# Performance work log

Hardware: AMD Instinct MI355X
Metric: run time of the kernel (lower is better)

Reference implementation:

```python
import jax, jax.numpy as jnp
import numpy as np

B, T, H = 64, 2048, 256
NEG_INF = -10.0 ** 10  # matches torch code's -10**10 pad value


def setup_inputs() -> dict:
    key = jax.random.key(0)
    k1, k2, k3, k4, k5 = jax.random.split(key, 5)
    questions = jax.random.normal(k1, (B, T, H), dtype=jnp.float32)
    questions_lens = jax.random.randint(k2, (B,), 1, T + 1)  # lengths in [1, T]
    W = jax.random.normal(k3, (H, H), dtype=jnp.float32) * (1.0 / np.sqrt(H))
    b = jax.random.normal(k4, (H,), dtype=jnp.float32) * 0.02
    v = jax.random.normal(k5, (H,), dtype=jnp.float32) * (1.0 / np.sqrt(H))
    return {"questions": questions, "questions_lens": questions_lens, "W": W, "b": b, "v": v}


def reference(questions, questions_lens, W, b, v):
    # energy[b,t] = v . (W @ q[b,t] + b)  -- batched instead of per-token loop
    # = (q @ W^T) @ v + (b . v)
    energies = jnp.einsum('bth,h->bt', jnp.einsum('bth,kh->btk', questions, W) + b, v)
    t_idx = jnp.arange(questions.shape[1])  # [T]
    mask = t_idx[None, :] < questions_lens[:, None]  # [B,T] valid positions
    energies = jnp.where(mask, energies, NEG_INF)
    return jax.nn.softmax(energies, axis=1)
```

## Files before the change

kernel.cpp:

```cpp
#include <hip/hip_runtime.h>

constexpr int B_ = 64;
constexpr int T_ = 2048;
constexpr int H_ = 256;
constexpr float NEGINF = -1e10f;

__global__ __launch_bounds__(256) void prep_kernel(
    const float* __restrict__ W, const float* __restrict__ v,
    float* __restrict__ partial) {
  const int h = threadIdx.x;
  const int j = blockIdx.x;
  float acc = 0.f;
#pragma unroll 8
  for (int kk = 0; kk < 64; ++kk) {
    const int k = j * 64 + kk;
    acc = fmaf(v[k], W[k * H_ + h], acc);
  }
  partial[j * H_ + h] = acc;
}

__global__ __launch_bounds__(256) void energy_kernel(
    const float4* __restrict__ q4, const int* __restrict__ lens,
    const float4* __restrict__ p4,
    float* __restrict__ e) {
  const int bb = blockIdx.y;
  const int t0 = blockIdx.x * 256;
  const int len = lens[bb];
  const int tid = threadIdx.x;
  float* erow = e + (size_t)bb * T_;

  if (t0 >= len) {
    erow[t0 + tid] = NEGINF;
    return;
  }

  const int tg = tid >> 3;
  const int c4 = tid & 7;

  float4 uf[8];
#pragma unroll
  for (int hh = 0; hh < 8; ++hh) {
    float4 s = p4[hh * 8 + c4];
#pragma unroll
    for (int j = 1; j < 4; ++j) {
      const float4 t = p4[j * 64 + hh * 8 + c4];
      s.x += t.x; s.y += t.y; s.z += t.z; s.w += t.w;
    }
    uf[hh] = s;
  }

  const float4* qbase =
      q4 + ((size_t)bb * T_ + t0 + tg) * (H_ / 4) + c4;

  float acc[8];
#pragma unroll
  for (int i = 0; i < 8; ++i) acc[i] = 0.f;

#pragma unroll
  for (int i = 0; i < 8; ++i) {
    const int t = t0 + tg + 32 * i;
    if (t < len) {
      const float4* qp = qbase + (size_t)i * 32 * (H_ / 4);
#pragma unroll
      for (int hh = 0; hh < 8; ++hh) {
        const float4 qv = qp[hh * 8];
        acc[i] = fmaf(qv.x, uf[hh].x, acc[i]);
        acc[i] = fmaf(qv.y, uf[hh].y, acc[i]);
        acc[i] = fmaf(qv.z, uf[hh].z, acc[i]);
        acc[i] = fmaf(qv.w, uf[hh].w, acc[i]);
      }
    }
  }

#pragma unroll
  for (int off = 1; off < 8; off <<= 1) {
#pragma unroll
    for (int i = 0; i < 8; ++i) acc[i] += __shfl_xor(acc[i], off);
  }

  float val = 0.f;
#pragma unroll
  for (int k = 0; k < 8; ++k)
    if (c4 == k) val = acc[k];
  const int t = t0 + tg + 32 * c4;
  erow[t] = (t < len) ? val : NEGINF;
}

__global__ __launch_bounds__(256) void softmax_kernel(
    const float* __restrict__ e, float* __restrict__ out) {
  const int bb = blockIdx.x;
  const int tid = threadIdx.x;
  const int wave = tid >> 6;
  const int lane = tid & 63;
  const float* erow = e + (size_t)bb * T_;
  float* orow = out + (size_t)bb * T_;

  float vals[T_ / 256];
  float m = NEGINF;
#pragma unroll
  for (int i = 0; i < T_ / 256; ++i) {
    vals[i] = erow[i * 256 + tid];
    m = fmaxf(m, vals[i]);
  }
#pragma unroll
  for (int off = 32; off > 0; off >>= 1) m = fmaxf(m, __shfl_xor(m, off));

  __shared__ float sm[4];
  __shared__ float ssum[4];
  if (lane == 0) sm[wave] = m;
  __syncthreads();
  m = fmaxf(fmaxf(sm[0], sm[1]), fmaxf(sm[2], sm[3]));

  float s = 0.f;
#pragma unroll
  for (int i = 0; i < T_ / 256; ++i) {
    vals[i] = expf(vals[i] - m);
    s += vals[i];
  }
#pragma unroll
  for (int off = 32; off > 0; off >>= 1) s += __shfl_xor(s, off);
  if (lane == 0) ssum[wave] = s;
  __syncthreads();
  s = ssum[0] + ssum[1] + ssum[2] + ssum[3];
  const float inv = 1.f / s;
#pragma unroll
  for (int i = 0; i < T_ / 256; ++i) orow[i * 256 + tid] = vals[i] * inv;
}

extern "C" void kernel_launch(void* const* d_in, const int* in_sizes, int n_in,
                              void* d_out, int out_size, void* d_ws,
                              size_t ws_size, hipStream_t stream) {
  const float* q = (const float*)d_in[0];
  const int* lens = (const int*)d_in[1];
  const float* W = (const float*)d_in[2];
  const float* v = (const float*)d_in[4];
  float* out = (float*)d_out;

  char* ws = (char*)d_ws;
  float* partial = (float*)ws;
  float* e = (float*)(ws + 8192);

  prep_kernel<<<dim3(4), dim3(256), 0, stream>>>(W, v, partial);
  energy_kernel<<<dim3(T_ / 256, B_), dim3(256), 0, stream>>>(
      (const float4*)q, lens, (const float4*)partial, e);
  softmax_kernel<<<dim3(B_), dim3(256), 0, stream>>>(e, out);
}
```

Before: 192.3 us.

## Fuse W^T v prep, energy and softmax into one kernel with last-block reduction

Merges the three kernels into a single launch. Each active block recomputes u = W^T v into shared memory, computes its tile of energies, then atomically bumps a per-row counter; the last block to finish a row does that row's softmax. A fast path drops per-row bounds checks for fully valid tiles. This removes two launches and inter-kernel gaps, but adds a memset, redundant W reads of 256 KB per active block, and a serial softmax tail on the last block of each row.

```diff
diff --git a/kernel.cpp b/kernel.cpp
--- a/kernel.cpp
+++ b/kernel.cpp
@@ -5,94 +5,99 @@
 constexpr int H_ = 256;
 constexpr float NEGINF = -1e10f;
 
-__global__ __launch_bounds__(256) void prep_kernel(
+__global__ __launch_bounds__(256) void fused_kernel(
+    const float4* __restrict__ q4, const int* __restrict__ lens,
     const float* __restrict__ W, const float* __restrict__ v,
-    float* __restrict__ partial) {
-  const int h = threadIdx.x;
-  const int j = blockIdx.x;
-  float acc = 0.f;
-#pragma unroll 8
-  for (int kk = 0; kk < 64; ++kk) {
-    const int k = j * 64 + kk;
-    acc = fmaf(v[k], W[k * H_ + h], acc);
-  }
-  partial[j * H_ + h] = acc;
-}
-
-__global__ __launch_bounds__(256) void energy_kernel(
-    const float4* __restrict__ q4, const int* __restrict__ lens,
-    const float4* __restrict__ p4,
-    float* __restrict__ e) {
+    float* __restrict__ e, unsigned int* __restrict__ row_cnt,
+    float* __restrict__ out) {
   const int bb = blockIdx.y;
   const int t0 = blockIdx.x * 256;
+  const int tid = threadIdx.x;
   const int len = lens[bb];
-  const int tid = threadIdx.x;
   float* erow = e + (size_t)bb * T_;
 
-  if (t0 >= len) {
+  __shared__ float su[H_];
+  __shared__ int s_last;
+
+  if (t0 < len) {
+    float uacc = 0.f;
+#pragma unroll 8
+    for (int k = 0; k < H_; ++k) uacc = fmaf(v[k], W[k * H_ + tid], uacc);
+    su[tid] = uacc;
+    __syncthreads();
+
+    const int tg = tid >> 3;
+    const int c4 = tid & 7;
+    float4 uf[8];
+#pragma unroll
+    for (int hh = 0; hh < 8; ++hh)
+      uf[hh] = reinterpret_cast<const float4*>(su)[hh * 8 + c4];
+
+    const float4* qbase =
+        q4 + ((size_t)bb * T_ + t0 + tg) * (H_ / 4) + c4;
+
+    float acc[8];
+#pragma unroll
+    for (int i = 0; i < 8; ++i) acc[i] = 0.f;
+
+    if (t0 + 256 <= len) {
+#pragma unroll
+      for (int i = 0; i < 8; ++i) {
+        const float4* qp = qbase + (size_t)i * 32 * (H_ / 4);
+#pragma unroll
+        for (int hh = 0; hh < 8; ++hh) {
+          const float4 qv = qp[hh * 8];
+          acc[i] = fmaf(qv.x, uf[hh].x, acc[i]);
+          acc[i] = fmaf(qv.y, uf[hh].y, acc[i]);
+          acc[i] = fmaf(qv.z, uf[hh].z, acc[i]);
+          acc[i] = fmaf(qv.w, uf[hh].w, acc[i]);
+        }
+      }
+    } else {
+#pragma unroll
+      for (int i = 0; i < 8; ++i) {
+        const int t = t0 + tg + 32 * i;
+        if (t < len) {
+          const float4* qp = qbase + (size_t)i * 32 * (H_ / 4);
+#pragma unroll
+          for (int hh = 0; hh < 8; ++hh) {
+            const float4 qv = qp[hh * 8];
+            acc[i] = fmaf(qv.x, uf[hh].x, acc[i]);
+            acc[i] = fmaf(qv.y, uf[hh].y, acc[i]);
+            acc[i] = fmaf(qv.z, uf[hh].z, acc[i]);
+            acc[i] = fmaf(qv.w, uf[hh].w, acc[i]);
+          }
+        }
+      }
+    }
+
+#pragma unroll
+    for (int off = 1; off < 8; off <<= 1) {
+#pragma unroll
+      for (int i = 0; i < 8; ++i) acc[i] += __shfl_xor(acc[i], off);
+    }
+
+    float val = 0.f;
+#pragma unroll
+    for (int k = 0; k < 8; ++k)
+      if (c4 == k) val = acc[k];
+    const int t = t0 + tg + 32 * c4;
+    erow[t] = (t < len) ? val : NEGINF;
+  } else {
     erow[t0 + tid] = NEGINF;
-    return;
   }
 
-  const int tg = tid >> 3;
-  const int c4 = tid & 7;
+  __threadfence();
+  if (tid == 0) {
+    const unsigned int old = atomicAdd(&row_cnt[bb], 1u);
+    s_last = (old == gridDim.x - 1) ? 1 : 0;
+  }
+  __syncthreads();
+  if (!s_last) return;
+  __threadfence();
 
-  float4 uf[8];
-#pragma unroll
-  for (int hh = 0; hh < 8; ++hh) {
-    float4 s = p4[hh * 8 + c4];
-#pragma unroll
-    for (int j = 1; j < 4; ++j) {
-      const float4 t = p4[j * 64 + hh * 8 + c4];
-      s.x += t.x; s.y += t.y; s.z += t.z; s.w += t.w;
-    }
-    uf[hh] = s;
-  }
-
-  const float4* qbase =
-      q4 + ((size_t)bb * T_ + t0 + tg) * (H_ / 4) + c4;
-
-  float acc[8];
-#pragma unroll
-  for (int i = 0; i < 8; ++i) acc[i] = 0.f;
-
-#pragma unroll
-  for (int i = 0; i < 8; ++i) {
-    const int t = t0 + tg + 32 * i;
-    if (t < len) {
-      const float4* qp = qbase + (size_t)i * 32 * (H_ / 4);
-#pragma unroll
-      for (int hh = 0; hh < 8; ++hh) {
-        const float4 qv = qp[hh * 8];
-        acc[i] = fmaf(qv.x, uf[hh].x, acc[i]);
-        acc[i] = fmaf(qv.y, uf[hh].y, acc[i]);
-        acc[i] = fmaf(qv.z, uf[hh].z, acc[i]);
-        acc[i] = fmaf(qv.w, uf[hh].w, acc[i]);
-      }
-    }
-  }
-
-#pragma unroll
-  for (int off = 1; off < 8; off <<= 1) {
-#pragma unroll
-    for (int i = 0; i < 8; ++i) acc[i] += __shfl_xor(acc[i], off);
-  }
-
-  float val = 0.f;
-#pragma unroll
-  for (int k = 0; k < 8; ++k)
-    if (c4 == k) val = acc[k];
-  const int t = t0 + tg + 32 * c4;
-  erow[t] = (t < len) ? val : NEGINF;
-}
-
-__global__ __launch_bounds__(256) void softmax_kernel(
-    const float* __restrict__ e, float* __restrict__ out) {
-  const int bb = blockIdx.x;
-  const int tid = threadIdx.x;
   const int wave = tid >> 6;
   const int lane = tid & 63;
-  const float* erow = e + (size_t)bb * T_;
   float* orow = out + (size_t)bb * T_;
 
   float vals[T_ / 256];
@@ -137,11 +142,12 @@
   float* out = (float*)d_out;
 
   char* ws = (char*)d_ws;
-  float* partial = (float*)ws;
-  float* e = (float*)(ws + 8192);
+  float* e = (float*)ws;
+  unsigned int* row_cnt =
+      (unsigned int*)(ws + (size_t)B_ * T_ * sizeof(float));
 
-  prep_kernel<<<dim3(4), dim3(256), 0, stream>>>(W, v, partial);
-  energy_kernel<<<dim3(T_ / 256, B_), dim3(256), 0, stream>>>(
-      (const float4*)q, lens, (const float4*)partial, e);
-  softmax_kernel<<<dim3(B_), dim3(256), 0, stream>>>(e, out);
+  hipMemsetAsync(row_cnt, 0, B_ * sizeof(unsigned int), stream);
+
+  fused_kernel<<<dim3(T_ / 256, B_), dim3(256), 0, stream>>>(
+      (const float4*)q, lens, W, v, e, row_cnt, (float*)d_out);
 }
```

After: 353.5 us. 1.84x slower.
